# Optimization experiments

Measured on AMD Instinct MI355X. Metric: run time of the kernel, lower is better.

Reference implementation:

```python
import jax, jax.numpy as jnp
import numpy as np
from jax import lax

BETA = 0.8
THRESHOLD = 1.0
SURROGATE_ALPHA = 4.0  # slope of sigmoid surrogate gradient
EPS = 1e-12            # matches torch F.normalize eps

@jax.custom_vjp
def surrogate_spike(m):
    # forward: hard threshold at THRESHOLD
    return (m >= THRESHOLD).astype(m.dtype)

def _spike_fwd(m):
    return surrogate_spike(m), m

def _spike_bwd(m, g):
    # sigmoid-derivative surrogate gradient around threshold
    s = jax.nn.sigmoid(SURROGATE_ALPHA * (m - THRESHOLD))
    return (g * SURROGATE_ALPHA * s * (1.0 - s),)

surrogate_spike.defvjp(_spike_fwd, _spike_bwd)

def _l2_normalize(x):
    n = jnp.sqrt(jnp.sum(x * x, axis=-1, keepdims=True))
    return x / jnp.maximum(n, EPS)

def setup_inputs() -> dict:
    key = jax.random.key(0)
    k1, k2, k3 = jax.random.split(key, 3)
    B, T, D, F = 4, 2048, 1024, 4096
    mlp_input = jax.random.normal(k1, (B, T, D), dtype=jnp.float32)
    mlp_activation = jax.random.normal(k2, (B, T, F), dtype=jnp.float32)
    W_proj = jax.random.normal(k3, (F, D), dtype=jnp.float32) * (1.0 / np.sqrt(D))
    theta = jnp.ones((F,), dtype=jnp.float32) * THRESHOLD
    return {"mlp_input": mlp_input, "mlp_activation": mlp_activation,
            "W_proj": W_proj, "theta": theta}

def reference(mlp_input, mlp_activation, W_proj, theta):
    B, T, D = mlp_input.shape
    Fdim = W_proj.shape[0]
    # gate_input: (B, T, d_ff) = mlp_input @ W^T
    gate_input = jnp.einsum('btd,fd->btf', mlp_input, W_proj)

    def step(mem, g_t):
        mem = BETA * mem + g_t               # leaky integrate
        spk = surrogate_spike(mem)           # fire
        mem = mem - theta * spk              # soft reset
        return mem, spk

    mem0 = jnp.zeros((B, Fdim), dtype=gate_input.dtype)
    # scan over time: (T, B, d_ff)
    _, spikes = lax.scan(step, mem0, jnp.swapaxes(gate_input, 0, 1))
    lif_gate = jnp.swapaxes(spikes, 0, 1)    # (B, T, d_ff)

    norm_mlp = _l2_normalize(mlp_activation)
    norm_lif = _l2_normalize(lif_gate)
    # cosine similarity of two (already) unit vectors == dot product
    cos = jnp.sum(norm_mlp * norm_lif, axis=-1)
    return 1.0 - jnp.mean(cos)
```

## Files before the change

### kernel.cpp

```cpp
#include <hip/hip_runtime.h>
#include <hip/hip_bf16.h>

typedef unsigned short u16;
typedef unsigned char  u8;
typedef unsigned int   u32;
typedef unsigned long long u64;
typedef __attribute__((ext_vector_type(4)))  int i32x4;
typedef __attribute__((ext_vector_type(16))) int i32x16;

#define T_LEN    2048
#define NB       4
#define K_DIM    1024
#define F_DIM    4096
#define M_FULL   (NB * T_LEN)
#define BETA_C   0.8f
#define THRESH_C 1.0f
#define S8DEC    (6.0f / 127.0f)
#define A_ENC    (127.0f / 6.0f)
#define W_ENC    (127.0f / 0.1875f)
#define C_QUANT  (0.1875f / 127.0f)

__device__ static inline u32 q8pack(float4 v, float s) {
    int q0 = (int)rintf(fminf(fmaxf(v.x * s, -127.f), 127.f));
    int q1 = (int)rintf(fminf(fmaxf(v.y * s, -127.f), 127.f));
    int q2 = (int)rintf(fminf(fmaxf(v.z * s, -127.f), 127.f));
    int q3 = (int)rintf(fminf(fmaxf(v.w * s, -127.f), 127.f));
    return (u32)(q0 & 255) | ((u32)(q1 & 255) << 8) | ((u32)(q2 & 255) << 16) |
           ((u32)(q3 & 255) << 24);
}

__global__ __launch_bounds__(256) void cvt8_kernel(const float* __restrict__ a,
                                                   const float* __restrict__ w,
                                                   u8* __restrict__ oa,
                                                   u8* __restrict__ ow,
                                                   int n4a, int n4tot) {
    int stride = gridDim.x * blockDim.x;
    for (int i = blockIdx.x * blockDim.x + threadIdx.x; i < n4tot; i += stride) {
        bool isA = (i < n4a);
        int j = isA ? i : (i - n4a);
        float4 v = isA ? ((const float4*)a)[j] : ((const float4*)w)[j];
        u32 p = q8pack(v, isA ? A_ENC : W_ENC);
        if (isA) ((u32*)oa)[j] = p; else ((u32*)ow)[j] = p;
    }
}

__device__ static inline void gload_lds16(const void* g, void* l) {
    __builtin_amdgcn_global_load_lds(
        (const __attribute__((address_space(1))) unsigned int*)g,
        (__attribute__((address_space(3))) unsigned int*)l, 16, 0, 0);
}

#define NT 16

__global__ __launch_bounds__(512, 2) void gemm_i8(const u8* __restrict__ A8,
                                                  const u8* __restrict__ W8,
                                                  u8* __restrict__ gateT) {
    __shared__ __attribute__((aligned(16))) char lbytes[65536];

    const int tid  = threadIdx.x;
    const int lane = tid & 63;
    const int w    = tid >> 6;
    const int wm   = w >> 2;
    const int wn   = w & 3;

    int orig = blockIdx.x;
    int wg   = (orig & 7) * 64 + (orig >> 3);
    const int bm = (wg >> 4) * 256;
    const int bn = (wg & 15) * 256;

    const u8* aG = A8 + (size_t)(bm + (tid & 255)) * K_DIM + (tid >> 8) * 16;
    const u8* wGp = W8 + (size_t)(bn + (tid & 255)) * K_DIM + (tid >> 8) * 16;

#define STAGE_T(dst, kt) {                                         \
    gload_lds16(aG + (kt),        (dst) + tid * 16);               \
    gload_lds16(aG + (kt) + 32,   (dst) + 8192 + tid * 16);        \
    gload_lds16(wGp + (kt),       (dst) + 16384 + tid * 16);       \
    gload_lds16(wGp + (kt) + 32,  (dst) + 24576 + tid * 16); }

    i32x16 acc[4][2] = {};
    i32x4 a[4], b[2];

#define LOAD_AB(ks)                                                              \
    _Pragma("unroll") for (int mf = 0; mf < 4; ++mf)                             \
        a[mf] = *(const i32x4*)(aptr + (ks) * 8192 + mf * 512);                  \
    _Pragma("unroll") for (int nf = 0; nf < 2; ++nf)                             \
        b[nf] = *(const i32x4*)(bptr + (ks) * 8192 + nf * 512);

#define MFMA8()                                                                  \
    asm volatile("s_waitcnt lgkmcnt(0)" ::: "memory");                           \
    __builtin_amdgcn_sched_barrier(0);                                           \
    __builtin_amdgcn_s_setprio(1);                                               \
    _Pragma("unroll") for (int mf = 0; mf < 4; ++mf)                             \
    _Pragma("unroll") for (int nf = 0; nf < 2; ++nf)                             \
        acc[mf][nf] = __builtin_amdgcn_mfma_i32_32x32x32_i8(                     \
            a[mf], b[nf], acc[mf][nf], 0, 0, 0);                                 \
    __builtin_amdgcn_s_setprio(0);

    STAGE_T(lbytes, 0);
    asm volatile("s_waitcnt vmcnt(0)" ::: "memory");
    __syncthreads();

    for (int t = 0; t < NT; ++t) {
        const int cur = t & 1;
        const char* aptr = lbytes + cur * 32768 + (lane >> 5) * 4096 +
                           (wm * 128 + (lane & 31)) * 16;
        const char* bptr = lbytes + cur * 32768 + 16384 + (lane >> 5) * 4096 +
                           (wn * 64 + (lane & 31)) * 16;
        char* dN = lbytes + (cur ^ 1) * 32768;
        const bool st = (t + 1 < NT);

        LOAD_AB(0);
        if (st) { STAGE_T(dN, (t + 1) * 64); }
        MFMA8();
        __builtin_amdgcn_s_barrier();

        LOAD_AB(1);
        MFMA8();
        if (st) { asm volatile("s_waitcnt vmcnt(0)" ::: "memory"); }
        __builtin_amdgcn_s_barrier();
    }

    u32* clw = (u32*)lbytes;
    const int hl = lane >> 5;
    const int cl = lane & 31;
#pragma unroll
    for (int mf = 0; mf < 4; ++mf)
#pragma unroll
        for (int nf = 0; nf < 2; ++nf) {
            int col = wn * 64 + nf * 32 + cl;
            int r4b = wm * 32 + mf * 8 + hl;
            i32x16 v = acc[mf][nf];
#pragma unroll
            for (int g = 0; g < 4; ++g) {
                int q0 = (int)rintf(fminf(fmaxf((float)v[4*g+0] * C_QUANT, -127.f), 127.f));
                int q1 = (int)rintf(fminf(fmaxf((float)v[4*g+1] * C_QUANT, -127.f), 127.f));
                int q2 = (int)rintf(fminf(fmaxf((float)v[4*g+2] * C_QUANT, -127.f), 127.f));
                int q3 = (int)rintf(fminf(fmaxf((float)v[4*g+3] * C_QUANT, -127.f), 127.f));
                u32 p = (u32)(q0 & 255) | ((u32)(q1 & 255) << 8) |
                        ((u32)(q2 & 255) << 16) | ((u32)(q3 & 255) << 24);
                int row4 = r4b + 2 * g;
                clw[col * 64 + (row4 ^ (col & 31))] = p;
            }
        }
    __syncthreads();
#pragma unroll
    for (int it = 0; it < 8; ++it) {
        int idx = tid + it * 512;
        int col = idx >> 4;
        int tof = idx & 15;
        u32 x0 = clw[col * 64 + ((tof * 4 + 0) ^ (col & 31))];
        u32 x1 = clw[col * 64 + ((tof * 4 + 1) ^ (col & 31))];
        u32 x2 = clw[col * 64 + ((tof * 4 + 2) ^ (col & 31))];
        u32 x3 = clw[col * 64 + ((tof * 4 + 3) ^ (col & 31))];
        uint4 q; q.x = x0; q.y = x1; q.z = x2; q.w = x3;
        *(uint4*)&gateT[(size_t)(bn + col) * M_FULL + bm + tof * 16] = q;
    }
#undef STAGE_T
#undef LOAD_AB
#undef MFMA8
}

__device__ static inline void lif_group(uint4 v, float& mem, float th,
                                        int lane, u64* pk, int tb, bool doout) {
    u32 ws[4] = {v.x, v.y, v.z, v.w};
#pragma unroll
    for (int w4 = 0; w4 < 4; ++w4) {
#pragma unroll
        for (int by = 0; by < 4; ++by) {
            int q = (int)((signed char)((ws[w4] >> (by * 8)) & 0xffu));
            mem = BETA_C * mem + (float)q * S8DEC;
            bool sp = (mem >= THRESH_C);
            u64 mk = __ballot(sp);
            if (sp) mem -= th;
            if (doout && lane == 0) pk[(size_t)(tb + w4 * 4 + by) * 64] = mk;
        }
    }
}

__global__ __launch_bounds__(256) void lif_kernel(const u8* __restrict__ gateT,
                                                  const float* __restrict__ theta,
                                                  u64* __restrict__ packed) {
    const int tid  = threadIdx.x;
    const int lane = tid & 63;
    const int wid  = blockIdx.x * 4 + (tid >> 6);
    const int fg   = wid & 63;
    const int s    = (wid >> 6) & 15;
    const int b    = wid >> 10;
    const int f    = fg * 64 + lane;
    const int m0   = b * T_LEN + s * 128;
    const float th = theta[f];
    const u8* gp = gateT + (size_t)f * M_FULL + m0;
    u64* pk = packed + (size_t)m0 * 64 + fg;
    float mem = 0.0f;

    if (s == 0) {
        uint4 v0 = *(const uint4*)(gp +   0), v1 = *(const uint4*)(gp +  16);
        uint4 v2 = *(const uint4*)(gp +  32), v3 = *(const uint4*)(gp +  48);
        uint4 v4 = *(const uint4*)(gp +  64), v5 = *(const uint4*)(gp +  80);
        uint4 v6 = *(const uint4*)(gp +  96), v7 = *(const uint4*)(gp + 112);
        lif_group(v0, mem, th, lane, pk,   0, true);
        lif_group(v1, mem, th, lane, pk,  16, true);
        lif_group(v2, mem, th, lane, pk,  32, true);
        lif_group(v3, mem, th, lane, pk,  48, true);
        lif_group(v4, mem, th, lane, pk,  64, true);
        lif_group(v5, mem, th, lane, pk,  80, true);
        lif_group(v6, mem, th, lane, pk,  96, true);
        lif_group(v7, mem, th, lane, pk, 112, true);
    } else {
        const u8* gw = gp - 64;
        uint4 w0 = *(const uint4*)(gw +   0), w1 = *(const uint4*)(gw +  16);
        uint4 w2 = *(const uint4*)(gw +  32), w3 = *(const uint4*)(gw +  48);
        uint4 v0 = *(const uint4*)(gp +   0), v1 = *(const uint4*)(gp +  16);
        uint4 v2 = *(const uint4*)(gp +  32), v3 = *(const uint4*)(gp +  48);
        uint4 v4 = *(const uint4*)(gp +  64), v5 = *(const uint4*)(gp +  80);
        uint4 v6 = *(const uint4*)(gp +  96), v7 = *(const uint4*)(gp + 112);
        lif_group(w0, mem, th, lane, pk, 0, false);
        lif_group(w1, mem, th, lane, pk, 0, false);
        lif_group(w2, mem, th, lane, pk, 0, false);
        lif_group(w3, mem, th, lane, pk, 0, false);
        lif_group(v0, mem, th, lane, pk,   0, true);
        lif_group(v1, mem, th, lane, pk,  16, true);
        lif_group(v2, mem, th, lane, pk,  32, true);
        lif_group(v3, mem, th, lane, pk,  48, true);
        lif_group(v4, mem, th, lane, pk,  64, true);
        lif_group(v5, mem, th, lane, pk,  80, true);
        lif_group(v6, mem, th, lane, pk,  96, true);
        lif_group(v7, mem, th, lane, pk, 112, true);
    }
}

__global__ __launch_bounds__(256) void row_reduce_kernel(const float* __restrict__ act,
                                                         const u64* __restrict__ packed,
                                                         float* __restrict__ row_cos) {
    int row = blockIdx.x;
    int tid = threadIdx.x;
    const float* a = act + (size_t)row * F_DIM + tid * 16;
    u64 wv = packed[(size_t)row * 64 + (tid >> 2)];
    unsigned bits = (unsigned)((wv >> ((tid & 3) * 16)) & 0xFFFFull);

    float dot = 0.f, a2 = 0.f;
    float cnt = (float)__popc(bits);
#pragma unroll
    for (int q = 0; q < 4; ++q) {
        float4 av = ((const float4*)a)[q];
        dot += ((bits >> (q * 4 + 0)) & 1) ? av.x : 0.f;
        dot += ((bits >> (q * 4 + 1)) & 1) ? av.y : 0.f;
        dot += ((bits >> (q * 4 + 2)) & 1) ? av.z : 0.f;
        dot += ((bits >> (q * 4 + 3)) & 1) ? av.w : 0.f;
        a2  += av.x * av.x + av.y * av.y + av.z * av.z + av.w * av.w;
    }
#pragma unroll
    for (int off = 32; off > 0; off >>= 1) {
        dot += __shfl_down(dot, off);
        a2  += __shfl_down(a2, off);
        cnt += __shfl_down(cnt, off);
    }
    __shared__ float sd[4], sa[4], sc[4];
    int w = tid >> 6, lane = tid & 63;
    if (lane == 0) { sd[w] = dot; sa[w] = a2; sc[w] = cnt; }
    __syncthreads();
    if (tid == 0) {
        float D  = sd[0] + sd[1] + sd[2] + sd[3];
        float A2 = sa[0] + sa[1] + sa[2] + sa[3];
        float Cn = sc[0] + sc[1] + sc[2] + sc[3];
        float na = fmaxf(sqrtf(A2), 1e-12f);
        float ns = fmaxf(sqrtf(Cn), 1e-12f);
        row_cos[row] = D / (na * ns);
    }
}

__global__ __launch_bounds__(256) void final_reduce_kernel(const float* __restrict__ row_cos,
                                                           float* __restrict__ out) {
    int tid = threadIdx.x;
    float sum = 0.f;
    for (int i = tid; i < M_FULL; i += 256) sum += row_cos[i];
#pragma unroll
    for (int off = 32; off > 0; off >>= 1) sum += __shfl_down(sum, off);
    __shared__ float sw[4];
    int w = tid >> 6, lane = tid & 63;
    if (lane == 0) sw[w] = sum;
    __syncthreads();
    if (tid == 0) out[0] = 1.0f - (sw[0] + sw[1] + sw[2] + sw[3]) * (1.0f / (float)M_FULL);
}

extern "C" void kernel_launch(void* const* d_in, const int* in_sizes, int n_in,
                              void* d_out, int out_size, void* d_ws, size_t ws_size,
                              hipStream_t stream) {
    const float* mlp_input = (const float*)d_in[0];
    const float* mlp_act   = (const float*)d_in[1];
    const float* W         = (const float*)d_in[2];
    const float* theta     = (const float*)d_in[3];
    float* out = (float*)d_out;

    char* ws = (char*)d_ws;
    size_t off = 0;
    auto alloc = [&](size_t n) { size_t o = off; off = (off + n + 255) & ~(size_t)255; return o; };

    u8* A8        = (u8*)(ws + alloc((size_t)M_FULL * K_DIM));
    u8* W8        = (u8*)(ws + alloc((size_t)F_DIM * K_DIM));
    u64* packed   = (u64*)(ws + alloc((size_t)M_FULL * 64 * 8));
    float* rowcos = (float*)(ws + alloc((size_t)M_FULL * 4));
    u8* gateT     = (u8*)(ws + alloc((size_t)F_DIM * M_FULL));

    const int n4a = M_FULL * K_DIM / 4;
    const int n4t = n4a + F_DIM * K_DIM / 4;
    cvt8_kernel<<<2048, 256, 0, stream>>>(mlp_input, W, A8, W8, n4a, n4t);

    gemm_i8<<<(M_FULL / 256) * (F_DIM / 256), 512, 0, stream>>>(A8, W8, gateT);

    lif_kernel<<<1024, 256, 0, stream>>>(gateT, theta, packed);

    row_reduce_kernel<<<M_FULL, 256, 0, stream>>>(mlp_act, packed, rowcos);
    final_reduce_kernel<<<1, 256, 0, stream>>>(rowcos, out);
}
```

Before: 128.9 us.

## Load GEMM operands directly from global into registers, dropping LDS staging

The int8 GEMM no longer stages A and W tiles through LDS with global_load_lds and barriers. Each wave now loads its MFMA fragments straight from global memory into registers, double-buffered, and the main loop has no barriers. LDS is kept only for the epilogue transpose. This trades away LDS reuse across waves, so A rows are fetched by 4 waves and W rows by 2, giving more global/L2 traffic and uncoalesced 16-byte strided loads in exchange for removing sync overhead.

```diff
diff --git a/kernel.cpp b/kernel.cpp
--- a/kernel.cpp
+++ b/kernel.cpp
@@ -44,18 +44,12 @@
     }
 }
 
-__device__ static inline void gload_lds16(const void* g, void* l) {
-    __builtin_amdgcn_global_load_lds(
-        (const __attribute__((address_space(1))) unsigned int*)g,
-        (__attribute__((address_space(3))) unsigned int*)l, 16, 0, 0);
-}
-
 #define NT 16
 
 __global__ __launch_bounds__(512, 2) void gemm_i8(const u8* __restrict__ A8,
                                                   const u8* __restrict__ W8,
                                                   u8* __restrict__ gateT) {
-    __shared__ __attribute__((aligned(16))) char lbytes[65536];
+    __shared__ __attribute__((aligned(16))) u32 clw[16384];
 
     const int tid  = threadIdx.x;
     const int lane = tid & 63;
@@ -68,59 +62,42 @@
     const int bm = (wg >> 4) * 256;
     const int bn = (wg & 15) * 256;
 
-    const u8* aG = A8 + (size_t)(bm + (tid & 255)) * K_DIM + (tid >> 8) * 16;
-    const u8* wGp = W8 + (size_t)(bn + (tid & 255)) * K_DIM + (tid >> 8) * 16;
-
-#define STAGE_T(dst, kt) {                                         \
-    gload_lds16(aG + (kt),        (dst) + tid * 16);               \
-    gload_lds16(aG + (kt) + 32,   (dst) + 8192 + tid * 16);        \
-    gload_lds16(wGp + (kt),       (dst) + 16384 + tid * 16);       \
-    gload_lds16(wGp + (kt) + 32,  (dst) + 24576 + tid * 16); }
+    const int khw = (lane >> 5) * 16;
+    const u8* aB = A8 + (size_t)(bm + wm * 128 + (lane & 31)) * K_DIM + khw;
+    const u8* bB = W8 + (size_t)(bn + wn * 64 + (lane & 31)) * K_DIM + khw;
 
     i32x16 acc[4][2] = {};
-    i32x4 a[4], b[2];
-
-#define LOAD_AB(ks)                                                              \
+    i32x4 aC[4][2], bC[2][2], aN[4][2], bN[2][2];
+
+#define LOADT(AR, BR, kt)                                                        \
+    _Pragma("unroll") for (int mf = 0; mf < 4; ++mf) {                           \
+        AR[mf][0] = *(const i32x4*)(aB + (size_t)mf * 32 * K_DIM + (kt));        \
+        AR[mf][1] = *(const i32x4*)(aB + (size_t)mf * 32 * K_DIM + (kt) + 32);   \
+    }                                                                            \
+    _Pragma("unroll") for (int nf = 0; nf < 2; ++nf) {                           \
+        BR[nf][0] = *(const i32x4*)(bB + (size_t)nf * 32 * K_DIM + (kt));        \
+        BR[nf][1] = *(const i32x4*)(bB + (size_t)nf * 32 * K_DIM + (kt) + 32);   \
+    }
+
+#define MFMAT(AR, BR)                                                            \
     _Pragma("unroll") for (int mf = 0; mf < 4; ++mf)                             \
-        a[mf] = *(const i32x4*)(aptr + (ks) * 8192 + mf * 512);                  \
-    _Pragma("unroll") for (int nf = 0; nf < 2; ++nf)                             \
-        b[nf] = *(const i32x4*)(bptr + (ks) * 8192 + nf * 512);
-
-#define MFMA8()                                                                  \
-    asm volatile("s_waitcnt lgkmcnt(0)" ::: "memory");                           \
-    __builtin_amdgcn_sched_barrier(0);                                           \
-    __builtin_amdgcn_s_setprio(1);                                               \
-    _Pragma("unroll") for (int mf = 0; mf < 4; ++mf)                             \
-    _Pragma("unroll") for (int nf = 0; nf < 2; ++nf)                             \
+    _Pragma("unroll") for (int nf = 0; nf < 2; ++nf) {                           \
         acc[mf][nf] = __builtin_amdgcn_mfma_i32_32x32x32_i8(                     \
-            a[mf], b[nf], acc[mf][nf], 0, 0, 0);                                 \
-    __builtin_amdgcn_s_setprio(0);
-
-    STAGE_T(lbytes, 0);
-    asm volatile("s_waitcnt vmcnt(0)" ::: "memory");
-    __syncthreads();
-
-    for (int t = 0; t < NT; ++t) {
-        const int cur = t & 1;
-        const char* aptr = lbytes + cur * 32768 + (lane >> 5) * 4096 +
-                           (wm * 128 + (lane & 31)) * 16;
-        const char* bptr = lbytes + cur * 32768 + 16384 + (lane >> 5) * 4096 +
-                           (wn * 64 + (lane & 31)) * 16;
-        char* dN = lbytes + (cur ^ 1) * 32768;
-        const bool st = (t + 1 < NT);
-
-        LOAD_AB(0);
-        if (st) { STAGE_T(dN, (t + 1) * 64); }
-        MFMA8();
-        __builtin_amdgcn_s_barrier();
-
-        LOAD_AB(1);
-        MFMA8();
-        if (st) { asm volatile("s_waitcnt vmcnt(0)" ::: "memory"); }
-        __builtin_amdgcn_s_barrier();
-    }
-
-    u32* clw = (u32*)lbytes;
+            AR[mf][0], BR[nf][0], acc[mf][nf], 0, 0, 0);                         \
+        acc[mf][nf] = __builtin_amdgcn_mfma_i32_32x32x32_i8(                     \
+            AR[mf][1], BR[nf][1], acc[mf][nf], 0, 0, 0);                         \
+    }
+
+    LOADT(aC, bC, 0);
+    for (int t = 0; t < NT; t += 2) {
+        LOADT(aN, bN, (t + 1) * 64);
+        MFMAT(aC, bC);
+        if (t + 2 < NT) { LOADT(aC, bC, (t + 2) * 64); }
+        MFMAT(aN, bN);
+    }
+#undef LOADT
+#undef MFMAT
+
     const int hl = lane >> 5;
     const int cl = lane & 31;
 #pragma unroll
@@ -155,9 +132,6 @@
         uint4 q; q.x = x0; q.y = x1; q.z = x2; q.w = x3;
         *(uint4*)&gateT[(size_t)(bn + col) * M_FULL + bm + tof * 16] = q;
     }
-#undef STAGE_T
-#undef LOAD_AB
-#undef MFMA8
 }
 
 __device__ static inline void lif_group(uint4 v, float& mem, float th,
```

Result: slower. 167.6 us (+30.0%).
